# Kernel tuning notes

Hardware: AMD Instinct MI355X
Metric: run time of the kernel (lower is better)

Reference implementation:

```python
import jax, jax.numpy as jnp
import numpy as np

VOCAB = 50257
EMBED = 256
NFREQ = 64
NRULES = 100
B, S = 4, 1024


def setup_inputs() -> dict:
    key = jax.random.key(0)
    ks = jax.random.split(key, 7)
    return {
        "token_ids": jax.random.randint(ks[0], (B, S), 0, VOCAB),
        "a_n": jax.random.normal(ks[1], (VOCAB, NFREQ), dtype=jnp.float32),
        "b_n": jax.random.normal(ks[2], (VOCAB, NFREQ), dtype=jnp.float32),
        "rule_transform": jax.random.normal(ks[3], (NRULES, EMBED, EMBED), dtype=jnp.float32),
        "token_rules": jax.random.randint(ks[4], (VOCAB,), 0, NRULES),
        "proj_w": jax.random.normal(ks[5], (EMBED, NFREQ), dtype=jnp.float32) * (1.0 / np.sqrt(NFREQ)),
        "proj_b": jax.random.normal(ks[6], (EMBED,), dtype=jnp.float32) * 0.01,
    }


def reference(token_ids, a_n, b_n, rule_transform, token_rules, proj_w, proj_b):
    vocab_size, nfreq = a_n.shape
    # fourier_freqs = linspace(1, F, F) -> [1..F]
    freqs = jnp.arange(1, nfreq + 1, dtype=jnp.float32)  # [F]
    x = token_ids.astype(jnp.float32)[..., None] / vocab_size  # [B,S,1]
    ang = (2.0 * jnp.pi) * freqs * x  # [B,S,F]
    # gather per-token fourier coefficients, fuse cos/sin combine
    fourier = a_n[token_ids] * jnp.cos(ang) + b_n[token_ids] * jnp.sin(ang)  # [B,S,F]
    base = jnp.einsum('bsf,df->bsd', fourier, proj_w) + proj_b  # [B,S,D]
    rule_idx = token_rules[token_ids]  # [B,S]
    rules = rule_transform[rule_idx]  # [B,S,D,D] gathered per token
    return jnp.einsum('bsd,bsde->bse', base, rules)  # [B,S,D]
```

## Files before the change

### kernel.cpp

```cpp
#include <hip/hip_runtime.h>
#include <math.h>

#define VOCAB   50257
#define EMBED   256
#define NFREQ   64
#define NRULES  100
#define NTOK    4096
#define CAP     256
#define CHUNK   16
#define NCHUNK  (CAP / CHUNK)

#define BASE_BYTES ((size_t)NTOK * EMBED * 4)
#define LIST_BYTES ((size_t)NRULES * CAP * 4)

__global__ __launch_bounds__(256) void prep_kernel(
    const float* __restrict__ proj_w,
    float*       __restrict__ wT,
    int*         __restrict__ counts)
{
    __shared__ float s_t[64 * 65];
    const int tid = threadIdx.x;
    const int b   = blockIdx.x;

    if (b == 0 && tid < NRULES) counts[tid] = 0;

    const float4* __restrict__ W4 =
        (const float4*)(proj_w + (size_t)b * 64 * NFREQ);
    #pragma unroll
    for (int i = 0; i < 4; ++i) {
        const int v = i * 256 + tid;
        const float4 w = W4[v];
        const int dl = v >> 4, f0 = (v & 15) * 4;
        s_t[dl * 65 + f0 + 0] = w.x;
        s_t[dl * 65 + f0 + 1] = w.y;
        s_t[dl * 65 + f0 + 2] = w.z;
        s_t[dl * 65 + f0 + 3] = w.w;
    }
    __syncthreads();
    #pragma unroll
    for (int j = 0; j < 16; ++j) {
        const int o = j * 256 + tid;
        const int f = o >> 6, c = o & 63;
        wT[f * EMBED + b * 64 + c] = s_t[c * 65 + f];
    }
}

__global__ __launch_bounds__(256) void fused_base_kernel(
    const int*   __restrict__ token_ids,
    const float* __restrict__ a_n,
    const float* __restrict__ b_n,
    const int*   __restrict__ token_rules,
    const float* __restrict__ wT,
    const float* __restrict__ proj_b,
    float*       __restrict__ base,
    int*         __restrict__ counts,
    int*         __restrict__ list)
{
    __shared__ float s_four[4][NFREQ];

    const int tid = threadIdx.x;
    const int tl  = tid >> 6;
    const int f   = tid & 63;
    const int tok_idx = blockIdx.x * 4 + tl;
    const int tok     = token_ids[tok_idx];

    const float x   = (float)tok * (1.0f / (float)VOCAB);
    const float rev = (float)(f + 1) * x;
    const float rf  = rev - floorf(rev);
    const float sv  = __builtin_amdgcn_sinf(rf);
    const float cv  = __builtin_amdgcn_cosf(rf);
    s_four[tl][f] = a_n[(size_t)tok * NFREQ + f] * cv
                  + b_n[(size_t)tok * NFREQ + f] * sv;

    if (f == 0) {
        const int rule = token_rules[tok];
        const int pos  = atomicAdd(&counts[rule], 1);
        if (pos < CAP) list[rule * CAP + pos] = tok_idx;
    }
    __syncthreads();

    const int   d    = tid;
    const float bias = proj_b[d];
    float a0 = bias, a1 = bias, a2 = bias, a3 = bias;

    #pragma unroll 4
    for (int q = 0; q < 16; ++q) {
        const float w0 = wT[(4 * q + 0) * EMBED + d];
        const float w1 = wT[(4 * q + 1) * EMBED + d];
        const float w2 = wT[(4 * q + 2) * EMBED + d];
        const float w3 = wT[(4 * q + 3) * EMBED + d];
        const float4 f0 = ((const float4*)s_four[0])[q];
        const float4 f1 = ((const float4*)s_four[1])[q];
        const float4 f2 = ((const float4*)s_four[2])[q];
        const float4 f3 = ((const float4*)s_four[3])[q];
        a0 += w0 * f0.x + w1 * f0.y + w2 * f0.z + w3 * f0.w;
        a1 += w0 * f1.x + w1 * f1.y + w2 * f1.z + w3 * f1.w;
        a2 += w0 * f2.x + w1 * f2.y + w2 * f2.z + w3 * f2.w;
        a3 += w0 * f3.x + w1 * f3.y + w2 * f3.z + w3 * f3.w;
    }
    base[(size_t)(blockIdx.x * 4 + 0) * EMBED + d] = a0;
    base[(size_t)(blockIdx.x * 4 + 1) * EMBED + d] = a1;
    base[(size_t)(blockIdx.x * 4 + 2) * EMBED + d] = a2;
    base[(size_t)(blockIdx.x * 4 + 3) * EMBED + d] = a3;
}

__global__ __launch_bounds__(512) void apply_kernel(
    const float* __restrict__ base,
    const float* __restrict__ rule_transform,
    const int*   __restrict__ counts,
    const int*   __restrict__ list,
    float*       __restrict__ out)
{
    __shared__ float s_mem[8192];

    const int rule = blockIdx.x;
    int cnt = counts[rule];
    if (cnt > CAP) cnt = CAP;
    const int t0 = blockIdx.y * CHUNK;
    if (t0 >= cnt) return;

    const int tid  = threadIdx.x;
    const int w8   = tid >> 6;
    const int ds   = w8 >> 1;
    const int eh   = w8 & 1;
    const int lane = tid & 63;

    const int* __restrict__ lst = list + rule * CAP;

    #pragma unroll
    for (int i = 0; i < 2; ++i) {
        const int v = i * 512 + tid;
        int tt = t0 + (v >> 6);
        if (tt > cnt - 1) tt = cnt - 1;
        const int row = lst[tt];
        ((float4*)s_mem)[v] =
            ((const float4*)(base + (size_t)row * EMBED))[v & 63];
    }
    __syncthreads();

    const float2* __restrict__ T2 =
        (const float2*)(rule_transform + (size_t)rule * EMBED * EMBED);
    const int d0 = ds * 64;
    const int ec = eh * 64 + lane;

    float2 acc[CHUNK];
    #pragma unroll
    for (int t = 0; t < CHUNK; ++t) { acc[t].x = 0.f; acc[t].y = 0.f; }

    float2 tv0[4], tv1[4], tvn[4];
    #pragma unroll
    for (int i = 0; i < 4; ++i) tv0[i] = T2[(size_t)(d0 + i) * 128 + ec];
    #pragma unroll
    for (int i = 0; i < 4; ++i) tv1[i] = T2[(size_t)(d0 + 4 + i) * 128 + ec];

    for (int dq = 0; dq < 16; ++dq) {
        if (dq < 14) {
            #pragma unroll
            for (int i = 0; i < 4; ++i)
                tvn[i] = T2[(size_t)(d0 + (dq + 2) * 4 + i) * 128 + ec];
        }
        #pragma unroll
        for (int t = 0; t < CHUNK; ++t) {
            const float4 b4 = *(const float4*)&s_mem[t * EMBED + d0 + dq * 4];
            acc[t].x += b4.x * tv0[0].x + b4.y * tv0[1].x
                      + b4.z * tv0[2].x + b4.w * tv0[3].x;
            acc[t].y += b4.x * tv0[0].y + b4.y * tv0[1].y
                      + b4.z * tv0[2].y + b4.w * tv0[3].y;
        }
        #pragma unroll
        for (int i = 0; i < 4; ++i) { tv0[i] = tv1[i]; tv1[i] = tvn[i]; }
    }

    __syncthreads();
    if (ds == 1 || ds == 3) {
        float2* dst = (float2*)(s_mem + ((ds >> 1) * 2 + eh) * 2048);
        #pragma unroll
        for (int t = 0; t < CHUNK; ++t) dst[t * 64 + lane] = acc[t];
    }
    __syncthreads();
    if (ds == 0 || ds == 2) {
        const float2* src = (const float2*)(s_mem + ((ds >> 1) * 2 + eh) * 2048);
        #pragma unroll
        for (int t = 0; t < CHUNK; ++t) {
            const float2 r = src[t * 64 + lane];
            acc[t].x += r.x; acc[t].y += r.y;
        }
    }
    __syncthreads();
    if (ds == 2) {
        float2* dst = (float2*)(s_mem + eh * 2048);
        #pragma unroll
        for (int t = 0; t < CHUNK; ++t) dst[t * 64 + lane] = acc[t];
    }
    __syncthreads();
    if (ds == 0) {
        const float2* src = (const float2*)(s_mem + eh * 2048);
        #pragma unroll
        for (int t = 0; t < CHUNK; ++t) {
            const float2 r = src[t * 64 + lane];
            acc[t].x += r.x; acc[t].y += r.y;
        }
        #pragma unroll
        for (int t = 0; t < CHUNK; ++t) {
            if (t0 + t < cnt) {
                const int row = lst[t0 + t];
                *(float2*)&out[(size_t)row * EMBED + eh * 128 + lane * 2] = acc[t];
            }
        }
    }
}

extern "C" void kernel_launch(void* const* d_in, const int* in_sizes, int n_in,
                              void* d_out, int out_size, void* d_ws, size_t ws_size,
                              hipStream_t stream) {
    const int*   token_ids      = (const int*)  d_in[0];
    const float* a_n            = (const float*)d_in[1];
    const float* b_n            = (const float*)d_in[2];
    const float* rule_transform = (const float*)d_in[3];
    const int*   token_rules    = (const int*)  d_in[4];
    const float* proj_w         = (const float*)d_in[5];
    const float* proj_b         = (const float*)d_in[6];
    float*       out            = (float*)d_out;

    float* base   = (float*)d_ws;
    int*   counts = (int*)((char*)d_ws + BASE_BYTES);
    int*   list   = (int*)((char*)d_ws + BASE_BYTES + 512);
    float* wT     = (float*)((char*)d_ws + BASE_BYTES + 512 + LIST_BYTES);

    prep_kernel<<<4, 256, 0, stream>>>(proj_w, wT, counts);
    fused_base_kernel<<<NTOK / 4, 256, 0, stream>>>(
        token_ids, a_n, b_n, token_rules, wT, proj_b, base, counts, list);
    apply_kernel<<<dim3(NRULES, NCHUNK), 512, 0, stream>>>(
        base, rule_transform, counts, list, out);
}
```

Measured before the change: 128.7 us.

## Stage base rows per wave and collapse the split-K reduction into one barrier

Each wave now loads only the 64-element slice of each token's base row that it needs into its own private shared-memory stage. This removes the block-wide barrier after the cooperative load. The four-way split-K reduction becomes a single write-then-sum step with one barrier instead of four, at the cost of more shared memory. The rule_transform prefetch also goes from two to three slices ahead, and token indices are held in scalar registers via readfirstlane. The larger LDS footprint and extra registers may lower occupancy, and the new base loads are scalar 4-byte loads rather than float4.

```diff
diff --git a/kernel.cpp b/kernel.cpp
--- a/kernel.cpp
+++ b/kernel.cpp
@@ -111,7 +111,8 @@
     const int*   __restrict__ list,
     float*       __restrict__ out)
 {
-    __shared__ float s_mem[8192];
+    __shared__ float s_stage[8 * CHUNK * 64];
+    __shared__ float s_part[6 * CHUNK * 128];
 
     const int rule = blockIdx.x;
     int cnt = counts[rule];
@@ -124,88 +125,77 @@
     const int ds   = w8 >> 1;
     const int eh   = w8 & 1;
     const int lane = tid & 63;
+    const int d0   = ds * 64;
 
     const int* __restrict__ lst = list + rule * CAP;
 
-    #pragma unroll
-    for (int i = 0; i < 2; ++i) {
-        const int v = i * 512 + tid;
-        int tt = t0 + (v >> 6);
+    int idx[CHUNK];
+    #pragma unroll
+    for (int t = 0; t < CHUNK; ++t) {
+        int tt = t0 + t;
         if (tt > cnt - 1) tt = cnt - 1;
-        const int row = lst[tt];
-        ((float4*)s_mem)[v] =
-            ((const float4*)(base + (size_t)row * EMBED))[v & 63];
-    }
-    __syncthreads();
+        idx[t] = __builtin_amdgcn_readfirstlane(lst[tt]);
+    }
+
+    float* my_stage = s_stage + w8 * (CHUNK * 64);
+    #pragma unroll
+    for (int t = 0; t < CHUNK; ++t)
+        my_stage[t * 64 + lane] = base[(size_t)idx[t] * EMBED + d0 + lane];
 
     const float2* __restrict__ T2 =
         (const float2*)(rule_transform + (size_t)rule * EMBED * EMBED);
-    const int d0 = ds * 64;
     const int ec = eh * 64 + lane;
 
     float2 acc[CHUNK];
     #pragma unroll
     for (int t = 0; t < CHUNK; ++t) { acc[t].x = 0.f; acc[t].y = 0.f; }
 
-    float2 tv0[4], tv1[4], tvn[4];
+    float2 tv0[4], tv1[4], tv2[4], tvn[4];
     #pragma unroll
     for (int i = 0; i < 4; ++i) tv0[i] = T2[(size_t)(d0 + i) * 128 + ec];
     #pragma unroll
     for (int i = 0; i < 4; ++i) tv1[i] = T2[(size_t)(d0 + 4 + i) * 128 + ec];
+    #pragma unroll
+    for (int i = 0; i < 4; ++i) tv2[i] = T2[(size_t)(d0 + 8 + i) * 128 + ec];
 
     for (int dq = 0; dq < 16; ++dq) {
-        if (dq < 14) {
+        if (dq < 13) {
             #pragma unroll
             for (int i = 0; i < 4; ++i)
-                tvn[i] = T2[(size_t)(d0 + (dq + 2) * 4 + i) * 128 + ec];
+                tvn[i] = T2[(size_t)(d0 + (dq + 3) * 4 + i) * 128 + ec];
         }
         #pragma unroll
         for (int t = 0; t < CHUNK; ++t) {
-            const float4 b4 = *(const float4*)&s_mem[t * EMBED + d0 + dq * 4];
+            const float4 b4 = *(const float4*)&my_stage[t * 64 + dq * 4];
             acc[t].x += b4.x * tv0[0].x + b4.y * tv0[1].x
                       + b4.z * tv0[2].x + b4.w * tv0[3].x;
             acc[t].y += b4.x * tv0[0].y + b4.y * tv0[1].y
                       + b4.z * tv0[2].y + b4.w * tv0[3].y;
         }
         #pragma unroll
-        for (int i = 0; i < 4; ++i) { tv0[i] = tv1[i]; tv1[i] = tvn[i]; }
-    }
-
-    __syncthreads();
-    if (ds == 1 || ds == 3) {
-        float2* dst = (float2*)(s_mem + ((ds >> 1) * 2 + eh) * 2048);
-        #pragma unroll
-        for (int t = 0; t < CHUNK; ++t) dst[t * 64 + lane] = acc[t];
-    }
-    __syncthreads();
-    if (ds == 0 || ds == 2) {
-        const float2* src = (const float2*)(s_mem + ((ds >> 1) * 2 + eh) * 2048);
-        #pragma unroll
-        for (int t = 0; t < CHUNK; ++t) {
-            const float2 r = src[t * 64 + lane];
-            acc[t].x += r.x; acc[t].y += r.y;
-        }
-    }
-    __syncthreads();
-    if (ds == 2) {
-        float2* dst = (float2*)(s_mem + eh * 2048);
+        for (int i = 0; i < 4; ++i) {
+            tv0[i] = tv1[i]; tv1[i] = tv2[i]; tv2[i] = tvn[i];
+        }
+    }
+
+    if (ds > 0) {
+        float2* dst = (float2*)(s_part + ((ds - 1) * 2 + eh) * (CHUNK * 128));
         #pragma unroll
         for (int t = 0; t < CHUNK; ++t) dst[t * 64 + lane] = acc[t];
     }
     __syncthreads();
     if (ds == 0) {
-        const float2* src = (const float2*)(s_mem + eh * 2048);
         #pragma unroll
         for (int t = 0; t < CHUNK; ++t) {
-            const float2 r = src[t * 64 + lane];
-            acc[t].x += r.x; acc[t].y += r.y;
-        }
-        #pragma unroll
-        for (int t = 0; t < CHUNK; ++t) {
-            if (t0 + t < cnt) {
-                const int row = lst[t0 + t];
-                *(float2*)&out[(size_t)row * EMBED + eh * 128 + lane * 2] = acc[t];
+            #pragma unroll
+            for (int r = 0; r < 3; ++r) {
+                const float2 p = ((const float2*)
+                    (s_part + (r * 2 + eh) * (CHUNK * 128)))[t * 64 + lane];
+                acc[t].x += p.x; acc[t].y += p.y;
             }
+            if (t0 + t < cnt)
+                *(float2*)&out[(size_t)idx[t] * EMBED + eh * 128 + lane * 2]
+                    = acc[t];
         }
     }
 }
```

Result: no change. 130.6 us (+1.4%).
